# Kernel tuning notes

Measured on AMD Instinct MI355X. Metric: run time of the kernel, lower is better.

## Reference

```python
import jax, jax.numpy as jnp
import numpy as np

DN = ('NCHW', 'OIHW', 'NCHW')


def setup_inputs() -> dict:
    key = jax.random.key(0)
    k1, k2, k3, k4 = jax.random.split(key, 4)
    B, C, H, W = 8, 64, 128, 416
    depth = jax.random.uniform(k1, (B, H, W), dtype=jnp.float32) * 10.0 + 1.0
    feat = jax.random.normal(k2, (B, C, H, W), dtype=jnp.float32)
    w1 = jax.random.normal(k3, (64, C, 3, 3), dtype=jnp.float32) * 0.05
    w2 = jax.random.normal(k4, (144, 64, 1, 1), dtype=jnp.float32) * 0.05
    return {"depth": depth, "feat": feat, "w1": w1, "w2": w2}


def reference(depth, feat, w1, w2):
    B, H, W = depth.shape
    S = 4  # 2 ** scale, scale=2
    # mask predictor: conv3x3 (no bias) -> relu -> conv1x1 (no bias)
    h = jax.lax.conv_general_dilated(feat, w1, (1, 1), ((1, 1), (1, 1)), dimension_numbers=DN)
    h = jax.nn.relu(h)
    mask = jax.lax.conv_general_dilated(h, w2, (1, 1), ((0, 0), (0, 0)), dimension_numbers=DN)
    # [B, 144, H, W] -> [B, 9, S, S, H, W], softmax over the 9 neighbor taps
    mask = mask.reshape(B, 9, S, S, H, W)
    mask = jax.nn.softmax(mask, axis=1)
    # unfold(depth, 3x3, pad=1): 9 shifted views, row-major (ky, kx) like torch
    pad = jnp.pad(depth, ((0, 0), (1, 1), (1, 1)))
    patches = jnp.stack([pad[:, ky:ky + H, kx:kx + W]
                         for ky in range(3) for kx in range(3)], axis=1)  # [B,9,H,W]
    up = jnp.sum(mask * patches[:, :, None, None], axis=1)  # [B,S,S,H,W]
    # pixel-shuffle: permute(0,3,1,4,2) -> [B,H,S,W,S] -> [B,S*H,S*W]
    out = up.transpose(0, 3, 1, 4, 2).reshape(B, S * H, S * W)
    return out
```

## Files before the change

### kernel.cpp

```cpp
#include <hip/hip_runtime.h>


using frag_ab = __attribute__((ext_vector_type(8))) short;
using frag_cd = __attribute__((ext_vector_type(4))) float;
typedef __attribute__((ext_vector_type(8))) unsigned short ushort8;

static __device__ __forceinline__ unsigned short f2bf(float f) {
    unsigned u = __builtin_bit_cast(unsigned, f);
    u += 0x7fff + ((u >> 16) & 1);
    return (unsigned short)(u >> 16);
}

__global__ void prep(const float* __restrict__ w1, const float* __restrict__ w2,
                     unsigned short* __restrict__ w1bf, unsigned short* __restrict__ w2bf,
                     unsigned short* __restrict__ nhwc, int do_pad) {
    int i = blockIdx.x * 256 + threadIdx.x;
    if (i < 36864) {
        int j = i & 7, oc = (i >> 3) & 63, g = i >> 9;
        int q = g & 3, kh = (g >> 2) & 1, tap = g >> 3;
        int ic = kh * 32 + q * 8 + j;
        w1bf[i] = f2bf(w1[(oc * 64 + ic) * 9 + (tap / 3) * 3 + (tap % 3)]);
    }
    if (i < 9216) {
        int j = i & 7, ch = (i >> 3) % 144, g = (i >> 3) / 144;
        int q = g & 3, kh = g >> 2;
        w2bf[i] = f2bf(w2[ch * 64 + (kh * 32 + q * 8 + j)]);
    }
    if (do_pad && i < 69888) {
        int b = i / 8736, rem = i - b * 8736;
        int pos = rem >> 3, pack = rem & 7;
        int row, w;
        if (pos < 836) { row = (pos < 418) ? 0 : 129; w = (pos < 418) ? pos : pos - 418; }
        else           { int t = pos - 836; row = 1 + (t >> 1); w = (t & 1) ? 417 : 0; }
        ushort8 z = {0, 0, 0, 0, 0, 0, 0, 0};
        *(ushort8*)&nhwc[(((size_t)b * 130 + row) * 418 + w) * 64 + pack * 8] = z;
    }
}

__global__ __launch_bounds__(256, 8) void nchw_to_nhwc(const float* __restrict__ feat,
                                                       unsigned short* __restrict__ nhwc) {
    __shared__ unsigned short sT[32 * 64];
    const int b = blockIdx.z, h = blockIdx.y, w0 = blockIdx.x * 32;
    const int tid = threadIdx.x;
    const int c = tid >> 2, j = tid & 3;
    const float* src = feat + (((size_t)b * 64 + c) * 128 + h) * 416 + w0 + j * 8;
    float4 v0 = *(const float4*)src;
    float4 v1 = *(const float4*)(src + 4);
    sT[(j * 8 + 0) * 64 + c] = f2bf(v0.x);
    sT[(j * 8 + 1) * 64 + c] = f2bf(v0.y);
    sT[(j * 8 + 2) * 64 + c] = f2bf(v0.z);
    sT[(j * 8 + 3) * 64 + c] = f2bf(v0.w);
    sT[(j * 8 + 4) * 64 + c] = f2bf(v1.x);
    sT[(j * 8 + 5) * 64 + c] = f2bf(v1.y);
    sT[(j * 8 + 6) * 64 + c] = f2bf(v1.z);
    sT[(j * 8 + 7) * 64 + c] = f2bf(v1.w);
    __syncthreads();
    const int w = tid >> 3, pack = tid & 7;
    ushort8 val = *(ushort8*)&sT[w * 64 + pack * 8];
    *(ushort8*)&nhwc[(((size_t)b * 130 + h + 1) * 418 + (w0 + w + 1)) * 64 + pack * 8] = val;
}

__global__ __launch_bounds__(256, 4) void convex_up_mfma2(
    const float* __restrict__ depth, const unsigned short* __restrict__ nhwc,
    const unsigned short* __restrict__ w1bf, const unsigned short* __restrict__ w2bf,
    float* __restrict__ out)
{
    constexpr int H = 128, W = 416, OW = 1664;
    constexpr int RS = 418 * 64;

    __shared__ __align__(16) unsigned short sF[1440 * 8];
    __shared__ float sD[180];

    const int tid  = threadIdx.x;
    const int wv   = tid >> 6;
    const int lane = tid & 63;
    const int q    = lane >> 4;
    const int ln   = lane & 15;
    const int bw = blockIdx.x, bh = blockIdx.y, b = blockIdx.z;
    const int h0 = bh * 8, w0 = bw * 16;

    if (tid < 180) {
        int lr = tid / 18, lc = tid % 18;
        int gh = h0 - 1 + lr, gw = w0 - 1 + lc;
        float v = 0.f;
        if ((unsigned)gh < (unsigned)H && (unsigned)gw < (unsigned)W)
            v = depth[((size_t)b * H + gh) * W + gw];
        sD[tid] = v;
    }

    const unsigned short* gbase = nhwc + ((size_t)(b * 130 + h0) * 418 + w0) * 64;
    #pragma unroll
    for (int k = 0; k < 6; ++k) {
        int i = wv + 4 * k;
        int c = i * 64 + lane;
        if (c < 1440) {
            int r = c / 144, m = c - r * 144;
            int col = m >> 3, iccs = m & 7;
            int icc = iccs ^ (col & 7);
            const unsigned short* g = gbase + (size_t)r * RS + col * 64 + icc * 8;
            __builtin_amdgcn_global_load_lds((const __attribute__((address_space(1))) void*)g,
                                             (__attribute__((address_space(3))) void*)&sF[c * 8],
                                             16, 0, 0);
        }
    }
    __syncthreads();

    frag_cd acc1[2][4];
    #pragma unroll
    for (int mt = 0; mt < 2; ++mt)
        #pragma unroll
        for (int nt = 0; nt < 4; ++nt) acc1[mt][nt] = frag_cd{0.f, 0.f, 0.f, 0.f};

    #pragma unroll
    for (int tap = 0; tap < 9; ++tap) {
        const int ky = tap / 3, kx = tap % 3;
        #pragma unroll
        for (int kh = 0; kh < 2; ++kh) {
            frag_ab a[2];
            #pragma unroll
            for (int mt = 0; mt < 2; ++mt) {
                int r = 2 * wv + mt + ky, col = ln + kx;
                int slot = (r * 18 + col) * 8 + ((kh * 4 + q) ^ (col & 7));
                a[mt] = *(const frag_ab*)&sF[slot * 8];
            }
            frag_ab bf[4];
            #pragma unroll
            for (int nt = 0; nt < 4; ++nt)
                bf[nt] = *(const frag_ab*)&w1bf[(size_t)((tap * 2 + kh) * 4 + q) * 512 + (nt * 16 + ln) * 8];
            #pragma unroll
            for (int mt = 0; mt < 2; ++mt)
                #pragma unroll
                for (int nt = 0; nt < 4; ++nt)
                    acc1[mt][nt] = __builtin_amdgcn_mfma_f32_16x16x32_bf16(a[mt], bf[nt], acc1[mt][nt], 0, 0, 0);
        }
    }

    __syncthreads();

    unsigned short* sH = sF + wv * 2304;
    #pragma unroll
    for (int mt = 0; mt < 2; ++mt)
        #pragma unroll
        for (int nt = 0; nt < 4; ++nt)
            #pragma unroll
            for (int r = 0; r < 4; ++r)
                sH[(mt * 16 + q * 4 + r) * 72 + nt * 16 + ln] = f2bf(fmaxf(acc1[mt][nt][r], 0.f));

    frag_cd acc2[2][9];
    #pragma unroll
    for (int mt = 0; mt < 2; ++mt)
        #pragma unroll
        for (int nt = 0; nt < 9; ++nt) acc2[mt][nt] = frag_cd{0.f, 0.f, 0.f, 0.f};

    #pragma unroll
    for (int kh = 0; kh < 2; ++kh) {
        frag_ab a2[2];
        #pragma unroll
        for (int mt = 0; mt < 2; ++mt)
            a2[mt] = *(const frag_ab*)&sH[(mt * 16 + ln) * 72 + kh * 32 + q * 8];
        #pragma unroll
        for (int nt = 0; nt < 9; ++nt) {
            frag_ab b2 = *(const frag_ab*)&w2bf[(size_t)((kh * 4 + q) * 144 + nt * 16 + ln) * 8];
            acc2[0][nt] = __builtin_amdgcn_mfma_f32_16x16x32_bf16(a2[0], b2, acc2[0][nt], 0, 0, 0);
            acc2[1][nt] = __builtin_amdgcn_mfma_f32_16x16x32_bf16(a2[1], b2, acc2[1][nt], 0, 0, 0);
        }
    }

    float* sOutw = (float*)sH;
    #pragma unroll
    for (int mt = 0; mt < 2; ++mt) {
        const int prow = 2 * wv + mt;
        #pragma unroll
        for (int r = 0; r < 4; ++r) {
            const int pcol = q * 4 + r;
            float lg[9];
            #pragma unroll
            for (int t = 0; t < 9; ++t) lg[t] = acc2[mt][t][r];
            float mx = lg[0];
            #pragma unroll
            for (int t = 1; t < 9; ++t) mx = fmaxf(mx, lg[t]);
            float sum = 0.f, up = 0.f;
            #pragma unroll
            for (int t = 0; t < 9; ++t) {
                float e = __expf(lg[t] - mx);
                sum += e;
                up  += e * sD[(prow + t / 3) * 18 + (pcol + t % 3)];
            }
            sOutw[(mt * 16 + pcol) * 17 + ln] = up / sum;
        }
    }
    float* outb = out + (size_t)b * 512 * OW + (size_t)(h0 + 2 * wv) * 4 * OW + w0 * 4;
    const int row_o = lane >> 3;
    const int mt_o  = row_o >> 2, sy_o = row_o & 3;
    #pragma unroll
    for (int v = 0; v < 2; ++v) {
        float4 o;
        #pragma unroll
        for (int e = 0; e < 4; ++e) {
            int j = (lane & 7) * 8 + v * 4 + e;
            o[e] = sOutw[(mt_o * 16 + (j >> 2)) * 17 + sy_o * 4 + (j & 3)];
        }
        *(float4*)&outb[(size_t)row_o * OW + (lane & 7) * 8 + v * 4] = o;
    }
}

__global__ __launch_bounds__(256, 3) void convex_up_mfma_fb(
    const float* __restrict__ depth, const float* __restrict__ feat,
    const unsigned short* __restrict__ w1bf, const unsigned short* __restrict__ w2bf,
    float* __restrict__ out)
{
    constexpr int H = 128, W = 416, OW = 1664;
    __shared__ unsigned short sF[8 * 10 * 18 * 8];
    __shared__ unsigned short sH[4][32 * 72];
    __shared__ float sD[10 * 18];
    const int tid = threadIdx.x, wv = tid >> 6, lane = tid & 63;
    const int q = lane >> 4, ln = lane & 15;
    const int bw = blockIdx.x, bh = blockIdx.y, b = blockIdx.z;
    const int h0 = bh * 8, w0 = bw * 16;
    if (tid < 180) {
        int lr = tid / 18, lc = tid % 18;
        int gh = h0 - 1 + lr, gw = w0 - 1 + lc;
        float v = 0.f;
        if ((unsigned)gh < (unsigned)H && (unsigned)gw < (unsigned)W)
            v = depth[((size_t)b * H + gh) * W + gw];
        sD[tid] = v;
    }
    for (int idx = tid; idx < 11520; idx += 256) {
        int ic = idx / 180, rem = idx - ic * 180;
        int lr = rem / 18, lc = rem - lr * 18;
        int gh = h0 - 1 + lr, gw = w0 - 1 + lc;
        float v = 0.f;
        if ((unsigned)gh < (unsigned)H && (unsigned)gw < (unsigned)W)
            v = feat[(((size_t)b * 64 + ic) * H + gh) * W + gw];
        sF[(((ic >> 3) * 10 + lr) * 18 + lc) * 8 + (ic & 7)] = f2bf(v);
    }
    __syncthreads();
    frag_cd acc1[2][4];
    for (int mt = 0; mt < 2; ++mt) for (int nt = 0; nt < 4; ++nt) acc1[mt][nt] = frag_cd{0.f,0.f,0.f,0.f};
    #pragma unroll
    for (int tap = 0; tap < 9; ++tap) {
        const int ky = tap / 3, kx = tap % 3;
        #pragma unroll
        for (int kh = 0; kh < 2; ++kh) {
            frag_ab a[2];
            #pragma unroll
            for (int mt = 0; mt < 2; ++mt)
                a[mt] = *(const frag_ab*)&sF[(((kh * 4 + q) * 10 + 2 * wv + mt + ky) * 18 + ln + kx) * 8];
            frag_ab bf[4];
            #pragma unroll
            for (int nt = 0; nt < 4; ++nt)
                bf[nt] = *(const frag_ab*)&w1bf[(size_t)((tap * 2 + kh) * 4 + q) * 512 + (nt * 16 + ln) * 8];
            #pragma unroll
            for (int mt = 0; mt < 2; ++mt)
                #pragma unroll
                for (int nt = 0; nt < 4; ++nt)
                    acc1[mt][nt] = __builtin_amdgcn_mfma_f32_16x16x32_bf16(a[mt], bf[nt], acc1[mt][nt], 0, 0, 0);
        }
    }
    #pragma unroll
    for (int mt = 0; mt < 2; ++mt)
        #pragma unroll
        for (int nt = 0; nt < 4; ++nt)
            #pragma unroll
            for (int r = 0; r < 4; ++r)
                sH[wv][(mt * 16 + q * 4 + r) * 72 + nt * 16 + ln] = f2bf(fmaxf(acc1[mt][nt][r], 0.f));
    frag_cd acc2[2][9];
    for (int mt = 0; mt < 2; ++mt) for (int nt = 0; nt < 9; ++nt) acc2[mt][nt] = frag_cd{0.f,0.f,0.f,0.f};
    #pragma unroll
    for (int kh = 0; kh < 2; ++kh) {
        frag_ab a2[2];
        #pragma unroll
        for (int mt = 0; mt < 2; ++mt)
            a2[mt] = *(const frag_ab*)&sH[wv][(mt * 16 + ln) * 72 + kh * 32 + q * 8];
        #pragma unroll
        for (int nt = 0; nt < 9; ++nt) {
            frag_ab b2 = *(const frag_ab*)&w2bf[(size_t)((kh * 4 + q) * 144 + nt * 16 + ln) * 8];
            acc2[0][nt] = __builtin_amdgcn_mfma_f32_16x16x32_bf16(a2[0], b2, acc2[0][nt], 0, 0, 0);
            acc2[1][nt] = __builtin_amdgcn_mfma_f32_16x16x32_bf16(a2[1], b2, acc2[1][nt], 0, 0, 0);
        }
    }
    float* sOutw = (float*)&sH[wv][0];
    #pragma unroll
    for (int mt = 0; mt < 2; ++mt) {
        const int prow = 2 * wv + mt;
        #pragma unroll
        for (int r = 0; r < 4; ++r) {
            const int pcol = q * 4 + r;
            float lg[9];
            #pragma unroll
            for (int t = 0; t < 9; ++t) lg[t] = acc2[mt][t][r];
            float mx = lg[0];
            #pragma unroll
            for (int t = 1; t < 9; ++t) mx = fmaxf(mx, lg[t]);
            float sum = 0.f, up = 0.f;
            #pragma unroll
            for (int t = 0; t < 9; ++t) {
                float e = __expf(lg[t] - mx);
                sum += e; up += e * sD[(prow + t / 3) * 18 + (pcol + t % 3)];
            }
            sOutw[(mt * 16 + pcol) * 17 + ln] = up / sum;
        }
    }
    float* outb = out + (size_t)b * 512 * OW + (size_t)(h0 + 2 * wv) * 4 * OW + w0 * 4;
    const int row_o = lane >> 3, mt_o = row_o >> 2, sy_o = row_o & 3;
    #pragma unroll
    for (int v = 0; v < 2; ++v) {
        float4 o;
        #pragma unroll
        for (int e = 0; e < 4; ++e) {
            int j = (lane & 7) * 8 + v * 4 + e;
            o[e] = sOutw[(mt_o * 16 + (j >> 2)) * 17 + sy_o * 4 + (j & 3)];
        }
        *(float4*)&outb[(size_t)row_o * OW + (lane & 7) * 8 + v * 4] = o;
    }
}

extern "C" void kernel_launch(void* const* d_in, const int* in_sizes, int n_in,
                              void* d_out, int out_size, void* d_ws, size_t ws_size,
                              hipStream_t stream) {
    const float* depth = (const float*)d_in[0];
    const float* feat  = (const float*)d_in[1];
    const float* w1    = (const float*)d_in[2];
    const float* w2    = (const float*)d_in[3];
    float* out = (float*)d_out;

    const size_t NHWC_USHORTS = (size_t)8 * 130 * 418 * 64;
    const size_t NEED = NHWC_USHORTS * 2 + (36864 + 9216) * 2;

    if (ws_size >= NEED) {
        unsigned short* nhwc = (unsigned short*)d_ws;
        unsigned short* w1bf = nhwc + NHWC_USHORTS;
        unsigned short* w2bf = w1bf + 36864;
        prep<<<273, 256, 0, stream>>>(w1, w2, w1bf, w2bf, nhwc, 1);
        nchw_to_nhwc<<<dim3(13, 128, 8), 256, 0, stream>>>(feat, nhwc);
        convex_up_mfma2<<<dim3(26, 16, 8), dim3(256), 0, stream>>>(depth, nhwc, w1bf, w2bf, out);
    } else {
        unsigned short* w1bf = (unsigned short*)d_ws;
        unsigned short* w2bf = w1bf + 36864;
        prep<<<273, 256, 0, stream>>>(w1, w2, w1bf, w2bf, nullptr, 0);
        convex_up_mfma_fb<<<dim3(26, 16, 8), dim3(256), 0, stream>>>(depth, feat, w1bf, w2bf, out);
    }
}
```

Baseline: 239.8 us.

## Double conv tile height to 16 rows and restructure NHWC transpose kernel

The main fused kernel now processes a 16x16 pixel tile with 512 threads (8 waves) instead of 8x16 with 256 threads. This shares the 3x3 halo rows across more output rows and halves the block count. The transpose kernel now handles two rows per block, packs channel pairs into 32-bit words, and uses a padded shared array to avoid bank conflicts. The unseen body of the main kernel must correctly index 8 waves and more rows. The bigger shared-memory footprint may also reduce occupancy.

```diff
diff --git a/kernel.cpp b/kernel.cpp
--- a/kernel.cpp
+++ b/kernel.cpp
@@ -9,6 +9,9 @@
     unsigned u = __builtin_bit_cast(unsigned, f);
     u += 0x7fff + ((u >> 16) & 1);
     return (unsigned short)(u >> 16);
+}
+static __device__ __forceinline__ unsigned int pkbf(float lo, float hi) {
+    return (unsigned int)f2bf(lo) | ((unsigned int)f2bf(hi) << 16);
 }
 
 __global__ void prep(const float* __restrict__ w1, const float* __restrict__ w2,
@@ -39,28 +42,37 @@
 
 __global__ __launch_bounds__(256, 8) void nchw_to_nhwc(const float* __restrict__ feat,
                                                        unsigned short* __restrict__ nhwc) {
-    __shared__ unsigned short sT[32 * 64];
-    const int b = blockIdx.z, h = blockIdx.y, w0 = blockIdx.x * 32;
+    __shared__ unsigned int sT[2][32 * 33];
+    const int b = blockIdx.z, h0 = blockIdx.y * 2, w0 = blockIdx.x * 32;
     const int tid = threadIdx.x;
-    const int c = tid >> 2, j = tid & 3;
-    const float* src = feat + (((size_t)b * 64 + c) * 128 + h) * 416 + w0 + j * 8;
-    float4 v0 = *(const float4*)src;
-    float4 v1 = *(const float4*)(src + 4);
-    sT[(j * 8 + 0) * 64 + c] = f2bf(v0.x);
-    sT[(j * 8 + 1) * 64 + c] = f2bf(v0.y);
-    sT[(j * 8 + 2) * 64 + c] = f2bf(v0.z);
-    sT[(j * 8 + 3) * 64 + c] = f2bf(v0.w);
-    sT[(j * 8 + 4) * 64 + c] = f2bf(v1.x);
-    sT[(j * 8 + 5) * 64 + c] = f2bf(v1.y);
-    sT[(j * 8 + 6) * 64 + c] = f2bf(v1.z);
-    sT[(j * 8 + 7) * 64 + c] = f2bf(v1.w);
+    const int cpair = tid >> 3;
+    const int wseg  = tid & 7;
+
+    #pragma unroll
+    for (int hh = 0; hh < 2; ++hh) {
+        const float* s0 = feat + (((size_t)b * 64 + 2 * cpair) * 128 + (h0 + hh)) * 416
+                               + w0 + wseg * 4;
+        float4 e = *(const float4*)s0;
+        float4 o = *(const float4*)(s0 + 416 * 128);
+        sT[hh][(wseg * 4 + 0) * 33 + cpair] = pkbf(e.x, o.x);
+        sT[hh][(wseg * 4 + 1) * 33 + cpair] = pkbf(e.y, o.y);
+        sT[hh][(wseg * 4 + 2) * 33 + cpair] = pkbf(e.z, o.z);
+        sT[hh][(wseg * 4 + 3) * 33 + cpair] = pkbf(e.w, o.w);
+    }
     __syncthreads();
-    const int w = tid >> 3, pack = tid & 7;
-    ushort8 val = *(ushort8*)&sT[w * 64 + pack * 8];
-    *(ushort8*)&nhwc[(((size_t)b * 130 + h + 1) * 418 + (w0 + w + 1)) * 64 + pack * 8] = val;
-}
-
-__global__ __launch_bounds__(256, 4) void convex_up_mfma2(
+    const int w = tid >> 3, j = tid & 7;
+    #pragma unroll
+    for (int hh = 0; hh < 2; ++hh) {
+        uint4 v;
+        v.x = sT[hh][w * 33 + j * 4 + 0];
+        v.y = sT[hh][w * 33 + j * 4 + 1];
+        v.z = sT[hh][w * 33 + j * 4 + 2];
+        v.w = sT[hh][w * 33 + j * 4 + 3];
+        *(uint4*)&nhwc[(((size_t)b * 130 + h0 + hh + 1) * 418 + (w0 + w + 1)) * 64 + j * 8] = v;
+    }
+}
+
+__global__ __launch_bounds__(512, 4) void convex_up_mfma3(
     const float* __restrict__ depth, const unsigned short* __restrict__ nhwc,
     const unsigned short* __restrict__ w1bf, const unsigned short* __restrict__ w2bf,
     float* __restrict__ out)
@@ -68,8 +80,8 @@
     constexpr int H = 128, W = 416, OW = 1664;
     constexpr int RS = 418 * 64;
 
-    __shared__ __align__(16) unsigned short sF[1440 * 8];
-    __shared__ float sD[180];
+    __shared__ __align__(16) unsigned short sF[2592 * 8];
+    __shared__ float sD[18 * 18];
 
     const int tid  = threadIdx.x;
     const int wv   = tid >> 6;
@@ -77,9 +89,9 @@
     const int q    = lane >> 4;
     const int ln   = lane & 15;
     const int bw = blockIdx.x, bh = blockIdx.y, b = blockIdx.z;
-    const int h0 = bh * 8, w0 = bw * 16;
-
-    if (tid < 180) {
+    const int h0 = bh * 16, w0 = bw * 16;
+
+    if (tid < 324) {
         int lr = tid / 18, lc = tid % 18;
         int gh = h0 - 1 + lr, gw = w0 - 1 + lc;
         float v = 0.f;
@@ -91,9 +103,9 @@
     const unsigned short* gbase = nhwc + ((size_t)(b * 130 + h0) * 418 + w0) * 64;
     #pragma unroll
     for (int k = 0; k < 6; ++k) {
-        int i = wv + 4 * k;
+        int i = wv + 8 * k;
         int c = i * 64 + lane;
-        if (c < 1440) {
+        if (c < 2592) {
             int r = c / 144, m = c - r * 144;
             int col = m >> 3, iccs = m & 7;
             int icc = iccs ^ (col & 7);
@@ -332,12 +344,12 @@
         unsigned short* w1bf = nhwc + NHWC_USHORTS;
         unsigned short* w2bf = w1bf + 36864;
         prep<<<273, 256, 0, stream>>>(w1, w2, w1bf, w2bf, nhwc, 1);
-        nchw_to_nhwc<<<dim3(13, 128, 8), 256, 0, stream>>>(feat, nhwc);
-        convex_up_mfma2<<<dim3(26, 16, 8), dim3(256), 0, stream>>>(depth, nhwc, w1bf, w2bf, out);
+        nchw_to_nhwc<<<dim3(13, 64, 8), 256, 0, stream>>>(feat, nhwc);
+        convex_up_mfma3<<<dim3(26, 8, 8), dim3(512), 0, stream>>>(depth, nhwc, w1bf, w2bf, out);
     } else {
         unsigned short* w1bf = (unsigned short*)d_ws;
         unsigned short* w2bf = w1bf + 36864;
         prep<<<273, 256, 0, stream>>>(w1, w2, w1bf, w2bf, nullptr, 0);
-        convex_up_mfma_fb<<<dim3(26, 16, 8), dim3(256), 0, stream>>>(depth, feat, w1bf, w2bf, out);
-    }
-}
+        convex_up_mfma_fb<<<dim3(26, 16, 8), 256, 0, stream>>>(depth, feat, w1bf, w2bf, out);
+    }
+}
```

Result: no change. 239.9 us (+0.0%).
